# Optimization experiments

Measured on AMD Instinct MI355X. Metric: run time of the kernel, lower is better.

Reference implementation:

```python
import jax, jax.numpy as jnp
import numpy as np

TOP_K = 2

def setup_inputs() -> dict:
    key = jax.random.key(0)
    k1, k2 = jax.random.split(key)
    x = jax.random.normal(k1, (8, 4096, 4096), dtype=jnp.float32)
    gate_w = jax.random.normal(k2, (64, 4096), dtype=jnp.float32) * (1.0 / np.sqrt(4096))
    return {"x": x, "gate_w": gate_w}

def reference(x, gate_w):
    # logits: [B, S, E] = x @ gate_w.T (nn.Linear with bias=False)
    logits = jnp.einsum('bsd,ed->bse', x, gate_w)
    probs = jax.nn.softmax(logits, axis=-1)
    weights, indices = jax.lax.top_k(probs, TOP_K)  # [B,S,K] each
    weights = weights / jnp.sum(weights, axis=-1, keepdims=True)
    return (indices, weights, logits)
```

## Files before the change

### kernel.cpp

```cpp
#include <hip/hip_runtime.h>
#include <math.h>


#define DELTA  1e-3f
#define LS     68
#define WPLANE 262144

typedef __bf16 bf16x8 __attribute__((ext_vector_type(8)));
typedef float  f32x4  __attribute__((ext_vector_type(4)));

#define MFMA(a, b, c) __builtin_amdgcn_mfma_f32_16x16x32_bf16(a, b, c, 0, 0, 0)

__device__ __forceinline__ void split1(float x, unsigned short& h, unsigned short& l)
{
    const unsigned xb = __float_as_uint(x);
    const unsigned hb = xb & 0xffff0000u;
    h = (unsigned short)(hb >> 16);
    const float fl = x - __uint_as_float(hb);
    l = (unsigned short)(__float_as_uint(fl) >> 16);
}

__global__ __launch_bounds__(256)
void router_wconv(const float* __restrict__ w, unsigned short* __restrict__ wsp)
{
    const int i = (blockIdx.x * 256 + threadIdx.x) * 4;
    const float4 v = *(const float4*)(w + i);
    ushort4 h4, l4;
    split1(v.x, h4.x, l4.x);
    split1(v.y, h4.y, l4.y);
    split1(v.z, h4.z, l4.z);
    split1(v.w, h4.w, l4.w);
    *(ushort4*)(wsp + i)          = h4;
    *(ushort4*)(wsp + WPLANE + i) = l4;
}

__global__ __launch_bounds__(128, 2)
void router_pass1(const float* __restrict__ x,
                  const unsigned short* __restrict__ wsp,
                  float* __restrict__ out,
                  int* __restrict__ flags)
{
    __shared__ unsigned short a_hi[32 * 128];
    __shared__ unsigned short a_lo[32 * 128];
    __shared__ float l_lds[32 * LS];

    const int tid  = threadIdx.x;
    const int lane = tid & 63;
    const int wv   = tid >> 6;
    const int row0 = blockIdx.x * 32;

    const int fr = lane & 15;
    const int fk = (lane >> 4) << 3;

    f32x4 acc[4];
#pragma unroll
    for (int ct = 0; ct < 4; ++ct) {
        acc[ct][0] = 0.f; acc[ct][1] = 0.f; acc[ct][2] = 0.f; acc[ct][3] = 0.f;
    }

    const int arow = wv * 16 + fr;
    const unsigned asw = (unsigned)((arow & 7) << 4);
    const char* ahbase = (const char*)a_hi + arow * 256;
    const char* albase = (const char*)a_lo + arow * 256;

    const unsigned short* wb[4];
#pragma unroll
    for (int ct = 0; ct < 4; ++ct)
        wb[ct] = wsp + (size_t)(ct * 16 + fr) * 4096 + fk;

    float4 xv[8];
#pragma unroll
    for (int j = 0; j < 8; ++j) {
        const int f = j * 512 + tid * 4;
        const int r = f >> 7, k = f & 127;
        xv[j] = *(const float4*)(x + (size_t)(row0 + r) * 4096 + k);
    }

    for (int t = 0; t < 32; ++t) {
        __syncthreads();
#pragma unroll
        for (int j = 0; j < 8; ++j) {
            const int f = j * 512 + tid * 4;
            const int r = f >> 7, k = f & 127;
            const float4 v = xv[j];
            ushort4 h4, l4;
            split1(v.x, h4.x, l4.x);
            split1(v.y, h4.y, l4.y);
            split1(v.z, h4.z, l4.z);
            split1(v.w, h4.w, l4.w);
            const unsigned off = (unsigned)(r * 256) +
                                 (((unsigned)(k * 2)) ^ ((unsigned)((r & 7) << 4)));
            *(ushort4*)((char*)a_hi + off) = h4;
            *(ushort4*)((char*)a_lo + off) = l4;
        }
        __syncthreads();

        if (t < 31) {
            const int k0n = (t + 1) * 128;
#pragma unroll
            for (int j = 0; j < 8; ++j) {
                const int f = j * 512 + tid * 4;
                const int r = f >> 7, k = f & 127;
                xv[j] = *(const float4*)(x + (size_t)(row0 + r) * 4096 + k0n + k);
            }
        }

#pragma unroll
        for (int ks = 0; ks < 4; ++ks) {
            const unsigned kk = (unsigned)(ks * 32 + fk);
            const bf16x8 ah = *(const bf16x8*)(ahbase + ((kk * 2) ^ asw));
            const bf16x8 al = *(const bf16x8*)(albase + ((kk * 2) ^ asw));
#pragma unroll
            for (int ct = 0; ct < 4; ++ct) {
                const unsigned short* p = wb[ct] + (size_t)(t * 128 + ks * 32);
                const bf16x8 bh = *(const bf16x8*)(p);
                const bf16x8 bl = *(const bf16x8*)(p + WPLANE);
                acc[ct] = MFMA(ah, bh, acc[ct]);
                acc[ct] = MFMA(al, bh, acc[ct]);
                acc[ct] = MFMA(ah, bl, acc[ct]);
            }
        }
    }

#pragma unroll
    for (int ct = 0; ct < 4; ++ct) {
#pragma unroll
        for (int i = 0; i < 4; ++i) {
            l_lds[(wv * 16 + (lane >> 4) * 4 + i) * LS + ct * 16 + fr] = acc[ct][i];
        }
    }
    __syncthreads();

    {
        float* lg = out + 131072 + (size_t)row0 * 64;
#pragma unroll
        for (int j = 0; j < 4; ++j) {
            const int f = j * 512 + tid * 4;
            const int r = f >> 6, e = f & 63;
            const float4 v = *(const float4*)(&l_lds[r * LS + e]);
            *(float4*)(lg + f) = v;
        }
    }

    if (tid < 32) {
        const int r = tid;
        float b1 = -3.4e38f, b2 = -3.4e38f, b3 = -3.4e38f;
        int i1 = 0, i2 = 0;
        for (int eq = 0; eq < 16; ++eq) {
            const float4 v4 = *(const float4*)(&l_lds[r * LS + eq * 4]);
            const float vv[4] = {v4.x, v4.y, v4.z, v4.w};
#pragma unroll
            for (int j = 0; j < 4; ++j) {
                const float v = vv[j];
                const int   e = eq * 4 + j;
                if (v > b1)      { b3 = b2; b2 = b1; i2 = i1; b1 = v; i1 = e; }
                else if (v > b2) { b3 = b2; b2 = v; i2 = e; }
                else if (v > b3) { b3 = v; }
            }
        }
        const float g   = __expf(b2 - b1);
        const float inv = 1.0f / (1.0f + g);
        const size_t o  = (size_t)(row0 + r) * 2;
        out[o]     = (float)i1;
        out[o + 1] = (float)i2;
        out[65536 + o]     = inv;
        out[65536 + o + 1] = g * inv;
        flags[row0 + r] = ((b1 - b2 < DELTA) || (b2 - b3 < DELTA)) ? 1 : 0;
    }
}

__global__ __launch_bounds__(256, 2)
void router_pass2(const float* __restrict__ x,
                  const float* __restrict__ w,
                  float* __restrict__ out,
                  const int* __restrict__ flags)
{
    const int wv   = threadIdx.x >> 6;
    const int lane = threadIdx.x & 63;
    const int base = blockIdx.x * 64 + wv * 16;

    for (int r = 0; r < 16; ++r) {
        const int row = base + r;
        if (!flags[row]) continue;

        const float* lg = out + 131072 + (size_t)row * 64;
        const float my = lg[lane];
        float wval = my;

        int ec[4];
#pragma unroll
        for (int m = 0; m < 4; ++m) {
            float v = wval;
            int   id = lane;
            for (int off = 32; off; off >>= 1) {
                const float ov = __shfl_xor(v, off);
                const int   oi = __shfl_xor(id, off);
                if (ov > v || (ov == v && oi < id)) { v = ov; id = oi; }
            }
            ec[m] = id;
            if (lane == id) wval = -3.4e38f;
        }

        double s0 = 0.0, s1 = 0.0, s2 = 0.0, s3 = 0.0;
        const float* xr = x + (size_t)row * 4096;
        const float* w0 = w + (size_t)ec[0] * 4096;
        const float* w1 = w + (size_t)ec[1] * 4096;
        const float* w2 = w + (size_t)ec[2] * 4096;
        const float* w3 = w + (size_t)ec[3] * 4096;
        for (int k = lane; k < 4096; k += 64) {
            const double xd = (double)xr[k];
            s0 += xd * (double)w0[k];
            s1 += xd * (double)w1[k];
            s2 += xd * (double)w2[k];
            s3 += xd * (double)w3[k];
        }
        for (int off = 32; off; off >>= 1) {
            s0 += __shfl_xor(s0, off);
            s1 += __shfl_xor(s1, off);
            s2 += __shfl_xor(s2, off);
            s3 += __shfl_xor(s3, off);
        }

        if (lane == 0) {
            double v4[4] = { s0, s1, s2, s3 };
            int    id[4] = { ec[0], ec[1], ec[2], ec[3] };
#pragma unroll
            for (int a = 0; a < 3; ++a)
#pragma unroll
                for (int b = a + 1; b < 4; ++b)
                    if (v4[b] > v4[a] || (v4[b] == v4[a] && id[b] < id[a])) {
                        double tv = v4[a]; v4[a] = v4[b]; v4[b] = tv;
                        int    ti = id[a]; id[a] = id[b]; id[b] = ti;
                    }
            const double g   = exp(v4[1] - v4[0]);
            const double inv = 1.0 / (1.0 + g);
            const size_t o   = (size_t)row * 2;
            out[o]     = (float)id[0];
            out[o + 1] = (float)id[1];
            out[65536 + o]     = (float)inv;
            out[65536 + o + 1] = (float)(g * inv);
        }
    }
}

extern "C" void kernel_launch(void* const* d_in, const int* in_sizes, int n_in,
                              void* d_out, int out_size, void* d_ws, size_t ws_size,
                              hipStream_t stream) {
    const float* x = (const float*)d_in[0];
    const float* w = (const float*)d_in[1];
    float* out = (float*)d_out;
    int* flags = (int*)d_ws;
    unsigned short* wsp = (unsigned short*)((char*)d_ws + 131072);

    hipLaunchKernelGGL(router_wconv, dim3(256),  dim3(256), 0, stream, w, wsp);
    hipLaunchKernelGGL(router_pass1, dim3(1024), dim3(128), 0, stream, x, wsp, out, flags);
    hipLaunchKernelGGL(router_pass2, dim3(512),  dim3(256), 0, stream, x, w, out, flags);
}
```

Before: 885.6 us.

## Stream x tiles directly into LDS with double-buffered async loads and split on read

Pass1 now uses global_load_lds to copy raw fp32 x tiles into a double-buffered LDS region, replacing the register-staged load, split-and-store path. The bf16 hi/lo split moves to after the LDS read, done per MFMA fragment. Blocks grow to 256 threads covering 64 rows, using 64KB of LDS. This removes register staging and one of the two barriers per k-step so that loads can overlap the MFMAs, but the larger LDS footprint may limit occupancy. The k-loop no longer has a per-iteration __syncthreads, so each wave relies on the vmcnt waits and on reading only rows it loaded itself.

```diff
diff --git a/kernel.cpp b/kernel.cpp
--- a/kernel.cpp
+++ b/kernel.cpp
@@ -5,11 +5,16 @@
 #define DELTA  1e-3f
 #define LS     68
 #define WPLANE 262144
+#define NT     32
 
 typedef __bf16 bf16x8 __attribute__((ext_vector_type(8)));
 typedef float  f32x4  __attribute__((ext_vector_type(4)));
 
 #define MFMA(a, b, c) __builtin_amdgcn_mfma_f32_16x16x32_bf16(a, b, c, 0, 0, 0)
+
+#define GLL16(gp, lp) __builtin_amdgcn_global_load_lds(                          \
+    (const __attribute__((address_space(1))) unsigned*)(gp),                     \
+    (__attribute__((address_space(3))) unsigned*)(lp), 16, 0, 0)
 
 __device__ __forceinline__ void split1(float x, unsigned short& h, unsigned short& l)
 {
@@ -18,6 +23,35 @@
     h = (unsigned short)(hb >> 16);
     const float fl = x - __uint_as_float(hb);
     l = (unsigned short)(__float_as_uint(fl) >> 16);
+}
+
+__device__ __forceinline__ void split8(const f32x4 v0, const f32x4 v1,
+                                       bf16x8& ah, bf16x8& al)
+{
+    union U { bf16x8 v; unsigned u[4]; };
+    U h, l;
+    const unsigned a0 = __float_as_uint(v0[0]), a1 = __float_as_uint(v0[1]);
+    const unsigned a2 = __float_as_uint(v0[2]), a3 = __float_as_uint(v0[3]);
+    const unsigned b0 = __float_as_uint(v1[0]), b1 = __float_as_uint(v1[1]);
+    const unsigned b2 = __float_as_uint(v1[2]), b3 = __float_as_uint(v1[3]);
+    h.u[0] = (a0 >> 16) | (a1 & 0xffff0000u);
+    h.u[1] = (a2 >> 16) | (a3 & 0xffff0000u);
+    h.u[2] = (b0 >> 16) | (b1 & 0xffff0000u);
+    h.u[3] = (b2 >> 16) | (b3 & 0xffff0000u);
+    const float f0 = v0[0] - __uint_as_float(a0 & 0xffff0000u);
+    const float f1 = v0[1] - __uint_as_float(a1 & 0xffff0000u);
+    const float f2 = v0[2] - __uint_as_float(a2 & 0xffff0000u);
+    const float f3 = v0[3] - __uint_as_float(a3 & 0xffff0000u);
+    const float f4 = v1[0] - __uint_as_float(b0 & 0xffff0000u);
+    const float f5 = v1[1] - __uint_as_float(b1 & 0xffff0000u);
+    const float f6 = v1[2] - __uint_as_float(b2 & 0xffff0000u);
+    const float f7 = v1[3] - __uint_as_float(b3 & 0xffff0000u);
+    l.u[0] = (__float_as_uint(f0) >> 16) | (__float_as_uint(f1) & 0xffff0000u);
+    l.u[1] = (__float_as_uint(f2) >> 16) | (__float_as_uint(f3) & 0xffff0000u);
+    l.u[2] = (__float_as_uint(f4) >> 16) | (__float_as_uint(f5) & 0xffff0000u);
+    l.u[3] = (__float_as_uint(f6) >> 16) | (__float_as_uint(f7) & 0xffff0000u);
+    ah = h.v;
+    al = l.v;
 }
 
 __global__ __launch_bounds__(256)
@@ -34,23 +68,21 @@
     *(ushort4*)(wsp + WPLANE + i) = l4;
 }
 
-__global__ __launch_bounds__(128, 2)
+__global__ __launch_bounds__(256, 2)
 void router_pass1(const float* __restrict__ x,
                   const unsigned short* __restrict__ wsp,
                   float* __restrict__ out,
                   int* __restrict__ flags)
 {
-    __shared__ unsigned short a_hi[32 * 128];
-    __shared__ unsigned short a_lo[32 * 128];
-    __shared__ float l_lds[32 * LS];
+    __shared__ __align__(16) char smem[65536];
 
     const int tid  = threadIdx.x;
     const int lane = tid & 63;
     const int wv   = tid >> 6;
-    const int row0 = blockIdx.x * 32;
+    const int row0 = blockIdx.x * 64;
 
     const int fr = lane & 15;
-    const int fk = (lane >> 4) << 3;
+    const int fq = lane >> 4;
 
     f32x4 acc[4];
 #pragma unroll
@@ -58,61 +90,54 @@
         acc[ct][0] = 0.f; acc[ct][1] = 0.f; acc[ct][2] = 0.f; acc[ct][3] = 0.f;
     }
 
+    const int half  = lane >> 5;
+    const unsigned colb = (unsigned)((lane & 31) * 16);
+    const char* gsrc[8];
+    char*       lbas[8];
+#pragma unroll
+    for (int j = 0; j < 8; ++j) {
+        const int row = wv * 16 + 2 * j + half;
+        const unsigned swz = colb ^ ((unsigned)(row & 7) << 4);
+        gsrc[j] = (const char*)x + (size_t)(row0 + row) * 16384 + swz;
+        lbas[j] = smem + (wv * 8 + j) * 1024;
+    }
+
+    const unsigned short* wb[4];
+#pragma unroll
+    for (int ct = 0; ct < 4; ++ct)
+        wb[ct] = wsp + (size_t)(ct * 16 + fr) * 4096 + fq * 8;
+
     const int arow = wv * 16 + fr;
-    const unsigned asw = (unsigned)((arow & 7) << 4);
-    const char* ahbase = (const char*)a_hi + arow * 256;
-    const char* albase = (const char*)a_lo + arow * 256;
-
-    const unsigned short* wb[4];
-#pragma unroll
-    for (int ct = 0; ct < 4; ++ct)
-        wb[ct] = wsp + (size_t)(ct * 16 + fr) * 4096 + fk;
-
-    float4 xv[8];
-#pragma unroll
-    for (int j = 0; j < 8; ++j) {
-        const int f = j * 512 + tid * 4;
-        const int r = f >> 7, k = f & 127;
-        xv[j] = *(const float4*)(x + (size_t)(row0 + r) * 4096 + k);
-    }
-
-    for (int t = 0; t < 32; ++t) {
-        __syncthreads();
-#pragma unroll
-        for (int j = 0; j < 8; ++j) {
-            const int f = j * 512 + tid * 4;
-            const int r = f >> 7, k = f & 127;
-            const float4 v = xv[j];
-            ushort4 h4, l4;
-            split1(v.x, h4.x, l4.x);
-            split1(v.y, h4.y, l4.y);
-            split1(v.z, h4.z, l4.z);
-            split1(v.w, h4.w, l4.w);
-            const unsigned off = (unsigned)(r * 256) +
-                                 (((unsigned)(k * 2)) ^ ((unsigned)((r & 7) << 4)));
-            *(ushort4*)((char*)a_hi + off) = h4;
-            *(ushort4*)((char*)a_lo + off) = l4;
-        }
-        __syncthreads();
-
-        if (t < 31) {
-            const int k0n = (t + 1) * 128;
-#pragma unroll
-            for (int j = 0; j < 8; ++j) {
-                const int f = j * 512 + tid * 4;
-                const int r = f >> 7, k = f & 127;
-                xv[j] = *(const float4*)(x + (size_t)(row0 + r) * 4096 + k0n + k);
-            }
-        }
-
+    const unsigned aswz = (unsigned)((arow & 7) << 4);
+    const char* abase = smem + arow * 512;
+
+#pragma unroll
+    for (int j = 0; j < 8; ++j) GLL16(gsrc[j], lbas[j]);
+
+#pragma unroll 1
+    for (int t = 0; t < NT; ++t) {
+        if (t + 1 < NT) {
+            const size_t go = (size_t)(t + 1) * 512;
+            const int    bo = ((t + 1) & 1) * 32768;
+#pragma unroll
+            for (int j = 0; j < 8; ++j) GLL16(gsrc[j] + go, lbas[j] + bo);
+            asm volatile("s_waitcnt vmcnt(8)" ::: "memory");
+        } else {
+            asm volatile("s_waitcnt vmcnt(0)" ::: "memory");
+        }
+        __builtin_amdgcn_sched_barrier(0);
+
+        const char* bufc = abase + (t & 1) * 32768;
 #pragma unroll
         for (int ks = 0; ks < 4; ++ks) {
-            const unsigned kk = (unsigned)(ks * 32 + fk);
-            const bf16x8 ah = *(const bf16x8*)(ahbase + ((kk * 2) ^ asw));
-            const bf16x8 al = *(const bf16x8*)(albase + ((kk * 2) ^ asw));
+            const unsigned i0 = (unsigned)(ks * 128 + fq * 32);
+            const f32x4 v0 = *(const f32x4*)(bufc + ( i0        ^ aswz));
+            const f32x4 v1 = *(const f32x4*)(bufc + ((i0 + 16u) ^ aswz));
+            bf16x8 ah, al;
+            split8(v0, v1, ah, al);
 #pragma unroll
             for (int ct = 0; ct < 4; ++ct) {
-                const unsigned short* p = wb[ct] + (size_t)(t * 128 + ks * 32);
+                const unsigned short* p = wb[ct] + t * 128 + ks * 32;
                 const bf16x8 bh = *(const bf16x8*)(p);
                 const bf16x8 bl = *(const bf16x8*)(p + WPLANE);
                 acc[ct] = MFMA(ah, bh, acc[ct]);
@@ -122,11 +147,13 @@
         }
     }
 
+    __syncthreads();
+    float* l_lds = (float*)smem;
 #pragma unroll
     for (int ct = 0; ct < 4; ++ct) {
 #pragma unroll
         for (int i = 0; i < 4; ++i) {
-            l_lds[(wv * 16 + (lane >> 4) * 4 + i) * LS + ct * 16 + fr] = acc[ct][i];
+            l_lds[(wv * 16 + fq * 4 + i) * LS + ct * 16 + fr] = acc[ct][i];
         }
     }
     __syncthreads();
@@ -135,14 +162,14 @@
         float* lg = out + 131072 + (size_t)row0 * 64;
 #pragma unroll
         for (int j = 0; j < 4; ++j) {
-            const int f = j * 512 + tid * 4;
+            const int f = j * 1024 + tid * 4;
             const int r = f >> 6, e = f & 63;
             const float4 v = *(const float4*)(&l_lds[r * LS + e]);
             *(float4*)(lg + f) = v;
         }
     }
 
-    if (tid < 32) {
+    if (tid < 64) {
         const int r = tid;
         float b1 = -3.4e38f, b2 = -3.4e38f, b3 = -3.4e38f;
         int i1 = 0, i2 = 0;
@@ -252,7 +279,7 @@
     int* flags = (int*)d_ws;
     unsigned short* wsp = (unsigned short*)((char*)d_ws + 131072);
 
-    hipLaunchKernelGGL(router_wconv, dim3(256),  dim3(256), 0, stream, w, wsp);
-    hipLaunchKernelGGL(router_pass1, dim3(1024), dim3(128), 0, stream, x, wsp, out, flags);
-    hipLaunchKernelGGL(router_pass2, dim3(512),  dim3(256), 0, stream, x, w, out, flags);
-}
+    hipLaunchKernelGGL(router_wconv, dim3(256), dim3(256), 0, stream, w, wsp);
+    hipLaunchKernelGGL(router_pass1, dim3(512), dim3(256), 0, stream, x, wsp, out, flags);
+    hipLaunchKernelGGL(router_pass2, dim3(512), dim3(256), 0, stream, x, w, out, flags);
+}
```

Measured after the change: 874.4 us. Within noise of the previous version (-1.3%).
